# Optimization experiments

Hardware: AMD Instinct MI355X
Metric: run time of the kernel (lower is better)

Reference implementation:

```python
import jax, jax.numpy as jnp
import numpy as np
from math import sqrt

IN_DIM = 512
OUT_DIM = 512
MOD_DIM = 256
BATCH = 1024
EPS = 1e-8


def _uniform_param(key, shape, fan_in):
    # torch.rand in [0,1) then scaled to [-k, k) with k = sqrt(1/fan_in)
    k = sqrt(1.0 / fan_in)
    return jax.random.uniform(key, shape, dtype=jnp.float32, minval=-k, maxval=k)


def setup_inputs() -> dict:
    key = jax.random.key(0)
    k1, k2, k3, k4, k5, k6 = jax.random.split(key, 6)
    modulations = jax.random.normal(k1, (BATCH, MOD_DIM), dtype=jnp.float32)
    x = jax.random.normal(k2, (BATCH, IN_DIM), dtype=jnp.float32)
    weight = _uniform_param(k3, (OUT_DIM, IN_DIM), IN_DIM)      # main weight
    bias = _uniform_param(k4, (OUT_DIM,), IN_DIM)               # main bias
    # nn.Linear(modulation_dim, in_dim): weight [in_dim, mod_dim], bias [in_dim]
    mod_w = _uniform_param(k5, (IN_DIM, MOD_DIM), MOD_DIM)
    mod_b = _uniform_param(k6, (IN_DIM,), MOD_DIM)
    return {"modulations": modulations, "x": x, "weight": weight,
            "bias": bias, "mod_w": mod_w, "mod_b": mod_b}


def reference(modulations, x, weight, bias, mod_w, mod_b):
    # scales: [B, in_dim]
    scales = modulations @ mod_w.T + mod_b
    # weight_1: [B, out_dim, in_dim] = weight broadcast-scaled per sample
    w1 = weight[None, :, :] * scales[:, None, :]
    # NOTE: faithful to source: sum over axis -2 (the OUT dim), per-column L2 renorm
    w2 = w1 * jax.lax.rsqrt(jnp.sum(jnp.square(w1), axis=-2, keepdims=True) + EPS)
    # (x.unsqueeze(-2) @ w2.transpose(-2,-1)).squeeze(-2) + bias -> [B, out_dim]
    out = jnp.einsum("bi,boi->bo", x, w2) + bias
    return out
```

## Files before the change

kernel.cpp:

```cpp
#include <hip/hip_runtime.h>
#include <math.h>

#define B_DIM    1024
#define IN_DIMS  512
#define OUT_DIMS 512
#define MOD_DIM  256
#define EPS_F    1e-8f

typedef __attribute__((ext_vector_type(8))) short bf16x8;
typedef __attribute__((ext_vector_type(4))) float f32x4;

__device__ __forceinline__ unsigned short f2bf(float f) {
    union { float f; unsigned u; } c; c.f = f;
    unsigned r = c.u + 0x7fffu + ((c.u >> 16) & 1u);
    return (unsigned short)(r >> 16);
}
__device__ __forceinline__ float bf2f(unsigned short h) {
    union { float f; unsigned u; } c; c.u = ((unsigned)h) << 16;
    return c.f;
}

__device__ __forceinline__ void gload_lds16(const void* g, void* l) {
    __builtin_amdgcn_global_load_lds(
        (const __attribute__((address_space(1))) unsigned int*)g,
        (__attribute__((address_space(3))) unsigned int*)l, 16, 0, 0);
}

#define LP1 264
#define LP2 536

__global__ __launch_bounds__(256, 2) void k1_mod(
    const float* __restrict__ mods,
    const float* __restrict__ mod_w,
    const float* __restrict__ mod_b,
    const float* __restrict__ weight,
    const float* __restrict__ x,
    unsigned short* __restrict__ t_bf,
    unsigned short* __restrict__ wbf)
{
    __shared__ unsigned short Ah[32 * LP1], Al[32 * LP1];
    __shared__ unsigned short Bh[32 * LP1], Bl[32 * LP1];
    __shared__ float4 csm[32][8];
    __shared__ float colsum_s[32];

    const int tid = threadIdx.x;
    const int n0 = blockIdx.x * 32;
    const int m0 = blockIdx.y * 32;
    const int lane = tid & 63, wv = tid >> 6;
    const int wm = (wv >> 1) * 16, wn = (wv & 1) * 16;
    const int lr = lane & 15, lq = lane >> 4;

    #pragma unroll
    for (int i = 0; i < 8; i++) {
        const int id = tid + i * 256;
        const int r = id >> 6, c4 = id & 63;
        float4 v = *(const float4*)&mods[(m0 + r) * MOD_DIM + c4 * 4];
        ushort4 h, l;
        h.x = f2bf(v.x); l.x = f2bf(v.x - bf2f(h.x));
        h.y = f2bf(v.y); l.y = f2bf(v.y - bf2f(h.y));
        h.z = f2bf(v.z); l.z = f2bf(v.z - bf2f(h.z));
        h.w = f2bf(v.w); l.w = f2bf(v.w - bf2f(h.w));
        *(ushort4*)&Ah[r * LP1 + c4 * 4] = h;
        *(ushort4*)&Al[r * LP1 + c4 * 4] = l;
    }
    #pragma unroll
    for (int i = 0; i < 8; i++) {
        const int id = tid + i * 256;
        const int r = id >> 6, c4 = id & 63;
        float4 v = *(const float4*)&mod_w[(n0 + r) * MOD_DIM + c4 * 4];
        ushort4 h, l;
        h.x = f2bf(v.x); l.x = f2bf(v.x - bf2f(h.x));
        h.y = f2bf(v.y); l.y = f2bf(v.y - bf2f(h.y));
        h.z = f2bf(v.z); l.z = f2bf(v.z - bf2f(h.z));
        h.w = f2bf(v.w); l.w = f2bf(v.w - bf2f(h.w));
        *(ushort4*)&Bh[r * LP1 + c4 * 4] = h;
        *(ushort4*)&Bl[r * LP1 + c4 * 4] = l;
    }

    if (tid < 128) {
        const int row = blockIdx.y * 16 + blockIdx.x;
        float4 v = *(const float4*)&weight[row * IN_DIMS + tid * 4];
        ushort4 h;
        h.x = f2bf(v.x); h.y = f2bf(v.y); h.z = f2bf(v.z); h.w = f2bf(v.w);
        *(ushort4*)&wbf[row * IN_DIMS + tid * 4] = h;
    }

    float xv[4];
    {
        const int gn = n0 + wn + lr;
        #pragma unroll
        for (int rr = 0; rr < 4; rr++) {
            const int gm = m0 + wm + lq * 4 + rr;
            xv[rr] = x[gm * IN_DIMS + gn];
        }
    }

    {
        const int c4 = tid & 7, rr = tid >> 3;
        float4 acc = {0.f, 0.f, 0.f, 0.f};
        #pragma unroll
        for (int it = 0; it < 16; it++) {
            const int row = rr + 32 * it;
            float4 v = *(const float4*)&weight[row * IN_DIMS + n0 + c4 * 4];
            acc.x += v.x * v.x; acc.y += v.y * v.y;
            acc.z += v.z * v.z; acc.w += v.w * v.w;
        }
        csm[rr][c4] = acc;
    }
    __syncthreads();
    if (tid < 8) {
        float4 s = csm[0][tid];
        #pragma unroll
        for (int j = 1; j < 32; j++) {
            float4 v = csm[j][tid];
            s.x += v.x; s.y += v.y; s.z += v.z; s.w += v.w;
        }
        *(float4*)&colsum_s[tid * 4] = s;
    }

    f32x4 acc = {};
    #pragma unroll
    for (int kk = 0; kk < 256; kk += 32) {
        const int ko = kk + lq * 8;
        bf16x8 ah = *(bf16x8*)&Ah[(wm + lr) * LP1 + ko];
        bf16x8 al = *(bf16x8*)&Al[(wm + lr) * LP1 + ko];
        bf16x8 bh = *(bf16x8*)&Bh[(wn + lr) * LP1 + ko];
        bf16x8 bl = *(bf16x8*)&Bl[(wn + lr) * LP1 + ko];
        acc = __builtin_amdgcn_mfma_f32_16x16x32_bf16(ah, bh, acc, 0, 0, 0);
        acc = __builtin_amdgcn_mfma_f32_16x16x32_bf16(ah, bl, acc, 0, 0, 0);
        acc = __builtin_amdgcn_mfma_f32_16x16x32_bf16(al, bh, acc, 0, 0, 0);
    }
    __syncthreads();

    {
        const int ln = wn + lr;
        const int gn = n0 + ln;
        const float cs = colsum_s[ln];
        const float mb = mod_b[gn];
        #pragma unroll
        for (int rr = 0; rr < 4; rr++) {
            const int gm = m0 + wm + lq * 4 + rr;
            const float s = acc[rr] + mb;
            const float tv = xv[rr] * s * rsqrtf(s * s * cs + EPS_F);
            t_bf[gm * IN_DIMS + gn] = f2bf(tv);
        }
    }
}

__global__ __launch_bounds__(256, 2) void k2_out(
    const unsigned short* __restrict__ t_bf,
    const unsigned short* __restrict__ wbf,
    const float* __restrict__ bias,
    float* __restrict__ out)
{
    __shared__ unsigned short As[32 * LP2];
    __shared__ unsigned short Bs[32 * LP2];

    const int tid = threadIdx.x;
    const int n0 = blockIdx.x * 32;
    const int m0 = blockIdx.y * 32;
    const int lane = tid & 63, wv = tid >> 6;
    const int wm = (wv >> 1) * 16, wn = (wv & 1) * 16;
    const int lr = lane & 15, lq = lane >> 4;

    const float bv = bias[n0 + wn + lr];

    #pragma unroll
    for (int i = 0; i < 8; i++) {
        const int r = wv * 8 + i;
        gload_lds16(t_bf + (m0 + r) * IN_DIMS + lane * 8, &As[r * LP2]);
    }
    #pragma unroll
    for (int i = 0; i < 8; i++) {
        const int r = wv * 8 + i;
        gload_lds16(wbf + (n0 + r) * IN_DIMS + lane * 8, &Bs[r * LP2]);
    }
    __syncthreads();

    f32x4 acc = {};
    #pragma unroll
    for (int kk = 0; kk < 512; kk += 32) {
        const int ko = kk + lq * 8;
        bf16x8 a = *(bf16x8*)&As[(wm + lr) * LP2 + ko];
        bf16x8 b = *(bf16x8*)&Bs[(wn + lr) * LP2 + ko];
        acc = __builtin_amdgcn_mfma_f32_16x16x32_bf16(a, b, acc, 0, 0, 0);
    }

    {
        const int gn = n0 + wn + lr;
        #pragma unroll
        for (int rr = 0; rr < 4; rr++) {
            const int gm = m0 + wm + lq * 4 + rr;
            out[gm * OUT_DIMS + gn] = acc[rr] + bv;
        }
    }
}

extern "C" void kernel_launch(void* const* d_in, const int* in_sizes, int n_in,
                              void* d_out, int out_size, void* d_ws, size_t ws_size,
                              hipStream_t stream)
{
    const float* modulations = (const float*)d_in[0];
    const float* x           = (const float*)d_in[1];
    const float* weight      = (const float*)d_in[2];
    const float* bias        = (const float*)d_in[3];
    const float* mod_w       = (const float*)d_in[4];
    const float* mod_b       = (const float*)d_in[5];
    float* out = (float*)d_out;

    unsigned short* t_bf = (unsigned short*)d_ws;
    unsigned short* wbf  = (unsigned short*)d_ws + (1024 * 512);

    k1_mod<<<dim3(16, 32), 256, 0, stream>>>(
        modulations, mod_w, mod_b, weight, x, t_bf, wbf);

    k2_out<<<dim3(16, 32), 256, 0, stream>>>(
        t_bf, wbf, bias, out);
}
```

Measured before the change: 74.79 us.

## Hoist bf16 split and column norms into a prep kernel, DMA swizzled tiles

Adds a prep kernel that computes per-column weight square-sums as partial sums, converts weight to bf16, and splits modulations and mod_w into hi/lo bf16 halves in an XOR-swizzled layout, all once. Previously every k1 block redid this conversion and recomputed a 512-row column-norm reduction redundantly across its 32 y-blocks. k1 now pulls the pre-split tiles straight into LDS with global_load_lds, reads them through the swizzle to avoid bank conflicts, and sums eight partial norms. The cost is an extra kernel launch and a workspace round trip.

```diff
diff --git a/kernel.cpp b/kernel.cpp
--- a/kernel.cpp
+++ b/kernel.cpp
@@ -26,22 +26,86 @@
         (__attribute__((address_space(3))) unsigned int*)l, 16, 0, 0);
 }
 
-#define LP1 264
-#define LP2 536
-
-__global__ __launch_bounds__(256, 2) void k1_mod(
+
+__global__ __launch_bounds__(256) void k0_prep(
+    const float* __restrict__ weight,
     const float* __restrict__ mods,
     const float* __restrict__ mod_w,
+    unsigned short* __restrict__ wbf,
+    unsigned short* __restrict__ AhP, unsigned short* __restrict__ AlP,
+    unsigned short* __restrict__ BhP, unsigned short* __restrict__ BlP,
+    float* __restrict__ csp)
+{
+    __shared__ float4 csm[32][8];
+    const int tid = threadIdx.x;
+    const int bid = blockIdx.x;
+
+    if (bid < 128) {
+        const int g = bid & 15, p = bid >> 4;
+        const int c4 = tid & 7, rr = tid >> 3;
+        float4 acc = {0.f, 0.f, 0.f, 0.f};
+        #pragma unroll
+        for (int it = 0; it < 2; it++) {
+            const int row = p * 64 + rr + 32 * it;
+            float4 v = *(const float4*)&weight[row * IN_DIMS + g * 32 + c4 * 4];
+            acc.x += v.x * v.x; acc.y += v.y * v.y;
+            acc.z += v.z * v.z; acc.w += v.w * v.w;
+        }
+        csm[rr][c4] = acc;
+        __syncthreads();
+        if (tid < 8) {
+            float4 s = csm[0][tid];
+            #pragma unroll
+            for (int j = 1; j < 32; j++) {
+                float4 v = csm[j][tid];
+                s.x += v.x; s.y += v.y; s.z += v.z; s.w += v.w;
+            }
+            *(float4*)&csp[p * 512 + g * 32 + tid * 4] = s;
+        }
+    } else if (bid < 384) {
+        const int row = (bid - 128) * 2 + (tid >> 7);
+        const int c4 = tid & 127;
+        float4 v = *(const float4*)&weight[row * IN_DIMS + c4 * 4];
+        ushort4 h;
+        h.x = f2bf(v.x); h.y = f2bf(v.y); h.z = f2bf(v.z); h.w = f2bf(v.w);
+        *(ushort4*)&wbf[row * IN_DIMS + c4 * 4] = h;
+    } else if (bid < 640) {
+        const int f = (bid - 384) * 256 + tid;
+        const int r = f >> 6, c4 = f & 63;
+        float4 v = *(const float4*)&mods[r * MOD_DIM + c4 * 4];
+        ushort4 h, l;
+        h.x = f2bf(v.x); l.x = f2bf(v.x - bf2f(h.x));
+        h.y = f2bf(v.y); l.y = f2bf(v.y - bf2f(h.y));
+        h.z = f2bf(v.z); l.z = f2bf(v.z - bf2f(h.z));
+        h.w = f2bf(v.w); l.w = f2bf(v.w - bf2f(h.w));
+        const int sw = ((((c4 >> 1) ^ (r & 7)) << 3) + (c4 & 1) * 4);
+        *(ushort4*)&AhP[r * 256 + sw] = h;
+        *(ushort4*)&AlP[r * 256 + sw] = l;
+    } else {
+        const int f = (bid - 640) * 256 + tid;
+        const int r = f >> 6, c4 = f & 63;
+        float4 v = *(const float4*)&mod_w[r * MOD_DIM + c4 * 4];
+        ushort4 h, l;
+        h.x = f2bf(v.x); l.x = f2bf(v.x - bf2f(h.x));
+        h.y = f2bf(v.y); l.y = f2bf(v.y - bf2f(h.y));
+        h.z = f2bf(v.z); l.z = f2bf(v.z - bf2f(h.z));
+        h.w = f2bf(v.w); l.w = f2bf(v.w - bf2f(h.w));
+        const int sw = ((((c4 >> 1) ^ (r & 7)) << 3) + (c4 & 1) * 4);
+        *(ushort4*)&BhP[r * 256 + sw] = h;
+        *(ushort4*)&BlP[r * 256 + sw] = l;
+    }
+}
+
+__global__ __launch_bounds__(256, 2) void k1_mod(
+    const unsigned short* __restrict__ AhP, const unsigned short* __restrict__ AlP,
+    const unsigned short* __restrict__ BhP, const unsigned short* __restrict__ BlP,
+    const float* __restrict__ csp,
     const float* __restrict__ mod_b,
-    const float* __restrict__ weight,
     const float* __restrict__ x,
-    unsigned short* __restrict__ t_bf,
-    unsigned short* __restrict__ wbf)
-{
-    __shared__ unsigned short Ah[32 * LP1], Al[32 * LP1];
-    __shared__ unsigned short Bh[32 * LP1], Bl[32 * LP1];
-    __shared__ float4 csm[32][8];
-    __shared__ float colsum_s[32];
+    unsigned short* __restrict__ t_bf)
+{
+    __shared__ unsigned short AhL[32 * 256], AlL[32 * 256];
+    __shared__ unsigned short BhL[32 * 256], BlL[32 * 256];
 
     const int tid = threadIdx.x;
     const int n0 = blockIdx.x * 32;
@@ -51,102 +115,53 @@
     const int lr = lane & 15, lq = lane >> 4;
 
     #pragma unroll
-    for (int i = 0; i < 8; i++) {
-        const int id = tid + i * 256;
-        const int r = id >> 6, c4 = id & 63;
-        float4 v = *(const float4*)&mods[(m0 + r) * MOD_DIM + c4 * 4];
-        ushort4 h, l;
-        h.x = f2bf(v.x); l.x = f2bf(v.x - bf2f(h.x));
-        h.y = f2bf(v.y); l.y = f2bf(v.y - bf2f(h.y));
-        h.z = f2bf(v.z); l.z = f2bf(v.z - bf2f(h.z));
-        h.w = f2bf(v.w); l.w = f2bf(v.w - bf2f(h.w));
-        *(ushort4*)&Ah[r * LP1 + c4 * 4] = h;
-        *(ushort4*)&Al[r * LP1 + c4 * 4] = l;
-    }
-    #pragma unroll
-    for (int i = 0; i < 8; i++) {
-        const int id = tid + i * 256;
-        const int r = id >> 6, c4 = id & 63;
-        float4 v = *(const float4*)&mod_w[(n0 + r) * MOD_DIM + c4 * 4];
-        ushort4 h, l;
-        h.x = f2bf(v.x); l.x = f2bf(v.x - bf2f(h.x));
-        h.y = f2bf(v.y); l.y = f2bf(v.y - bf2f(h.y));
-        h.z = f2bf(v.z); l.z = f2bf(v.z - bf2f(h.z));
-        h.w = f2bf(v.w); l.w = f2bf(v.w - bf2f(h.w));
-        *(ushort4*)&Bh[r * LP1 + c4 * 4] = h;
-        *(ushort4*)&Bl[r * LP1 + c4 * 4] = l;
-    }
-
-    if (tid < 128) {
-        const int row = blockIdx.y * 16 + blockIdx.x;
-        float4 v = *(const float4*)&weight[row * IN_DIMS + tid * 4];
-        ushort4 h;
-        h.x = f2bf(v.x); h.y = f2bf(v.y); h.z = f2bf(v.z); h.w = f2bf(v.w);
-        *(ushort4*)&wbf[row * IN_DIMS + tid * 4] = h;
-    }
-
+    for (int i = 0; i < 4; i++) {
+        const int pr = wv * 8 + 2 * i;
+        gload_lds16(AhP + (m0 + pr) * 256 + lane * 8, &AhL[pr * 256]);
+        gload_lds16(AlP + (m0 + pr) * 256 + lane * 8, &AlL[pr * 256]);
+        gload_lds16(BhP + (n0 + pr) * 256 + lane * 8, &BhL[pr * 256]);
+        gload_lds16(BlP + (n0 + pr) * 256 + lane * 8, &BlL[pr * 256]);
+    }
+
+    const int gn = n0 + wn + lr;
     float xv[4];
-    {
-        const int gn = n0 + wn + lr;
-        #pragma unroll
-        for (int rr = 0; rr < 4; rr++) {
-            const int gm = m0 + wm + lq * 4 + rr;
-            xv[rr] = x[gm * IN_DIMS + gn];
-        }
-    }
-
-    {
-        const int c4 = tid & 7, rr = tid >> 3;
-        float4 acc = {0.f, 0.f, 0.f, 0.f};
-        #pragma unroll
-        for (int it = 0; it < 16; it++) {
-            const int row = rr + 32 * it;
-            float4 v = *(const float4*)&weight[row * IN_DIMS + n0 + c4 * 4];
-            acc.x += v.x * v.x; acc.y += v.y * v.y;
-            acc.z += v.z * v.z; acc.w += v.w * v.w;
-        }
-        csm[rr][c4] = acc;
-    }
+    #pragma unroll
+    for (int rr = 0; rr < 4; rr++)
+        xv[rr] = x[(m0 + wm + lq * 4 + rr) * IN_DIMS + gn];
+    float pp[8];
+    #pragma unroll
+    for (int p = 0; p < 8; p++)
+        pp[p] = csp[p * 512 + gn];
+    const float mb = mod_b[gn];
+
     __syncthreads();
-    if (tid < 8) {
-        float4 s = csm[0][tid];
-        #pragma unroll
-        for (int j = 1; j < 32; j++) {
-            float4 v = csm[j][tid];
-            s.x += v.x; s.y += v.y; s.z += v.z; s.w += v.w;
-        }
-        *(float4*)&colsum_s[tid * 4] = s;
-    }
 
     f32x4 acc = {};
     #pragma unroll
     for (int kk = 0; kk < 256; kk += 32) {
         const int ko = kk + lq * 8;
-        bf16x8 ah = *(bf16x8*)&Ah[(wm + lr) * LP1 + ko];
-        bf16x8 al = *(bf16x8*)&Al[(wm + lr) * LP1 + ko];
-        bf16x8 bh = *(bf16x8*)&Bh[(wn + lr) * LP1 + ko];
-        bf16x8 bl = *(bf16x8*)&Bl[(wn + lr) * LP1 + ko];
+        const int sw = ((ko >> 3) ^ (lr & 7)) << 3;
+        bf16x8 ah = *(bf16x8*)&AhL[(wm + lr) * 256 + sw];
+        bf16x8 al = *(bf16x8*)&AlL[(wm + lr) * 256 + sw];
+        bf16x8 bh = *(bf16x8*)&BhL[(wn + lr) * 256 + sw];
+        bf16x8 bl = *(bf16x8*)&BlL[(wn + lr) * 256 + sw];
         acc = __builtin_amdgcn_mfma_f32_16x16x32_bf16(ah, bh, acc, 0, 0, 0);
         acc = __builtin_amdgcn_mfma_f32_16x16x32_bf16(ah, bl, acc, 0, 0, 0);
         acc = __builtin_amdgcn_mfma_f32_16x16x32_bf16(al, bh, acc, 0, 0, 0);
     }
-    __syncthreads();
-
-    {
-        const int ln = wn + lr;
-        const int gn = n0 + ln;
-        const float cs = colsum_s[ln];
-        const float mb = mod_b[gn];
-        #pragma unroll
-        for (int rr = 0; rr < 4; rr++) {
-            const int gm = m0 + wm + lq * 4 + rr;
-            const float s = acc[rr] + mb;
-            const float tv = xv[rr] * s * rsqrtf(s * s * cs + EPS_F);
-            t_bf[gm * IN_DIMS + gn] = f2bf(tv);
-        }
-    }
-}
-
+
+    const float cs = ((pp[0] + pp[1]) + (pp[2] + pp[3]))
+                   + ((pp[4] + pp[5]) + (pp[6] + pp[7]));
+    #pragma unroll
+    for (int rr = 0; rr < 4; rr++) {
+        const int gm = m0 + wm + lq * 4 + rr;
+        const float s = acc[rr] + mb;
+        const float tv = xv[rr] * s * rsqrtf(s * s * cs + EPS_F);
+        t_bf[gm * IN_DIMS + gn] = f2bf(tv);
+    }
+}
+
+#define LP2 536
 __global__ __launch_bounds__(256, 2) void k2_out(
     const unsigned short* __restrict__ t_bf,
     const unsigned short* __restrict__ wbf,
@@ -208,11 +223,20 @@
     const float* mod_b       = (const float*)d_in[5];
     float* out = (float*)d_out;
 
-    unsigned short* t_bf = (unsigned short*)d_ws;
-    unsigned short* wbf  = (unsigned short*)d_ws + (1024 * 512);
+    char* ws = (char*)d_ws;
+    unsigned short* t_bf = (unsigned short*)(ws);
+    unsigned short* wbf  = (unsigned short*)(ws + (1u << 20));
+    unsigned short* AhP  = (unsigned short*)(ws + (3u << 19));
+    unsigned short* AlP  = (unsigned short*)(ws + (4u << 19));
+    unsigned short* BhP  = (unsigned short*)(ws + (5u << 19));
+    unsigned short* BlP  = (unsigned short*)(ws + (11u << 18));
+    float*          csp  = (float*)         (ws + (3u << 20));
+
+    k0_prep<<<dim3(768), 256, 0, stream>>>(
+        weight, modulations, mod_w, wbf, AhP, AlP, BhP, BlP, csp);
 
     k1_mod<<<dim3(16, 32), 256, 0, stream>>>(
-        modulations, mod_w, mod_b, weight, x, t_bf, wbf);
+        AhP, AlP, BhP, BlP, csp, mod_b, x, t_bf);
 
     k2_out<<<dim3(16, 32), 256, 0, stream>>>(
         t_bf, wbf, bias, out);
```

Result: slower. 76.52 us (+2.3%).
